# Kernel tuning notes

Measured on AMD Instinct MI355X. Metric: run time of the kernel, lower is better.

## Reference

```python
import jax, jax.numpy as jnp
import numpy as np

NUM_HEADS = 16
HEAD_DIM = 72
SCALE = HEAD_DIM ** -0.5
EPS = 1e-12


def l2norm(t):
    # torch F.normalize(dim=-1): x / norm.clamp_min(eps)
    n = jnp.sqrt(jnp.sum(t * t, axis=-1, keepdims=True))
    return t / jnp.maximum(n, EPS)


def setup_inputs() -> dict:
    key = jax.random.key(0)
    ks = jax.random.split(key, 7)
    B, N, C = 8, 1024, 1152
    x = jax.random.normal(ks[0], (B, N, C), dtype=jnp.float32)
    k_dino = jax.random.normal(ks[1], (B, NUM_HEADS, N, HEAD_DIM), dtype=jnp.float32)
    v_dino = jax.random.normal(ks[2], (B, NUM_HEADS, N, HEAD_DIM), dtype=jnp.float32)
    W_qkv = jax.random.normal(ks[3], (C, 3 * C), dtype=jnp.float32) * (C ** -0.5)
    b_qkv = jax.random.normal(ks[4], (3 * C,), dtype=jnp.float32) * 0.01
    W_proj = jax.random.normal(ks[5], (C, C), dtype=jnp.float32) * (C ** -0.5)
    b_proj = jax.random.normal(ks[6], (C,), dtype=jnp.float32) * 0.01
    return {"x": x, "k_dino": k_dino, "v_dino": v_dino,
            "W_qkv": W_qkv, "b_qkv": b_qkv, "W_proj": W_proj, "b_proj": b_proj}


def reference(x, k_dino, v_dino, W_qkv, b_qkv, W_proj, b_proj):
    # Stage 2, align_mode='logits_attn' (default path)
    B, N, C = x.shape
    qkv = (x @ W_qkv + b_qkv).reshape(B, N, 3, NUM_HEADS, HEAD_DIM)
    qkv = jnp.transpose(qkv, (2, 0, 3, 1, 4))  # [3, B, H, N, hd]
    q, k_sit, v_sit = qkv[0], qkv[1], qkv[2]   # qk_norm=False -> Identity

    # dual Q@K^T logits
    logits_dino = jnp.einsum('bhnd,bhmd->bhnm', q, k_dino) * SCALE
    logits_sit = jnp.einsum('bhnd,bhmd->bhnm', q, k_sit) * SCALE
    logits_dino_n = l2norm(logits_dino)
    logits_sit_n = l2norm(logits_sit)
    # cosine_similarity of already-unit vectors == dot product
    logit_align_loss = 1.0 - jnp.mean(jnp.sum(logits_sit_n * jax.lax.stop_gradient(logits_dino_n), axis=-1))

    attn_w_dino = jax.nn.softmax(logits_dino, axis=-1)
    attn_w_sit = jax.nn.softmax(logits_sit, axis=-1)
    attn_dino = jnp.einsum('bhnm,bhmd->bhnd', attn_w_dino, v_dino)
    attn_sit = jnp.einsum('bhnm,bhmd->bhnd', attn_w_sit, v_sit)
    attn_sit_n = l2norm(attn_sit)
    attn_dino_n = l2norm(attn_dino)
    attn_align_loss = 1.0 - jnp.mean(jnp.sum(attn_sit_n * jax.lax.stop_gradient(attn_dino_n), axis=-1))

    distill_loss = 1.0 * logit_align_loss + 0.5 * attn_align_loss

    # main attention path uses k_sit/v_sit -> identical math to attn_sit
    out = jnp.transpose(attn_sit, (0, 2, 1, 3)).reshape(B, N, C)
    out = out @ W_proj + b_proj
    return out, distill_loss
```

## Files before the change

kernel.cpp:

```cpp
#include <hip/hip_runtime.h>
#include <hip/hip_bf16.h>

typedef unsigned short bf_t;
typedef __attribute__((ext_vector_type(8))) short short8;
typedef __attribute__((ext_vector_type(4))) float f32x4;

#define B_ 8
#define H_ 16
#define N_ 1024
#define C_ 1152
#define HD 72
#define SCALE_F 0.11785113019775793f
#define EPS_F 1e-12f

typedef const __attribute__((address_space(1))) void* gas_p;
typedef __attribute__((address_space(3))) void* las_p;

__device__ inline bf_t f2bf(float f) {
  union { __hip_bfloat16 h; bf_t u; } cv;
  cv.h = __float2bfloat16(f);
  return cv.u;
}

__device__ inline void glds16(const bf_t* g, bf_t* l) {
  __builtin_amdgcn_global_load_lds((gas_p)g, (las_p)l, 16, 0, 0);
}

__global__ __launch_bounds__(256) void cast_bf16_k(const float* __restrict__ in,
                                                   bf_t* __restrict__ out, int n4) {
  int i = blockIdx.x * 256 + threadIdx.x;
  if (i < n4) {
    float4 v = reinterpret_cast<const float4*>(in)[i];
    ushort4 o;
    o.x = f2bf(v.x); o.y = f2bf(v.y); o.z = f2bf(v.z); o.w = f2bf(v.w);
    reinterpret_cast<ushort4*>(out)[i] = o;
  }
}

__global__ __launch_bounds__(256) void transpose_cast_k(const float* __restrict__ in,
                                                        bf_t* __restrict__ out, int R, int C) {
  __shared__ float t[32][33];
  const size_t bo = (size_t)blockIdx.z * R * C;
  const int tx = threadIdx.x, ty = threadIdx.y;
  const int r0 = blockIdx.y * 32, c0 = blockIdx.x * 32;
#pragma unroll
  for (int i = 0; i < 4; ++i) {
    int r = r0 + ty + i * 8, c = c0 + tx;
    if (r < R && c < C) t[ty + i * 8][tx] = in[bo + (size_t)r * C + c];
  }
  __syncthreads();
#pragma unroll
  for (int i = 0; i < 4; ++i) {
    int c = c0 + ty + i * 8, r = r0 + tx;
    if (r < R && c < C) out[bo + (size_t)c * R + r] = f2bf(t[tx][ty + i * 8]);
  }
}

template <int EPI>
__global__ __launch_bounds__(256) void gemm_bt_k(
    const bf_t* __restrict__ A, const bf_t* __restrict__ Bt,
    const float* __restrict__ bias, int K,
    bf_t* __restrict__ q_out, bf_t* __restrict__ k_out, bf_t* __restrict__ vT_out,
    float* __restrict__ f_out, int ldc) {
  __shared__ bf_t Alds[128 * 32];
  __shared__ bf_t Blds[128 * 32];
  const int tid = threadIdx.x, lane = tid & 63, wave = tid >> 6;
  const int l15 = lane & 15, l4 = lane >> 4;
  const int m0 = blockIdx.x * 128, n0 = blockIdx.y * 128;
  const int wr = (wave >> 1) * 64, wc = (wave & 1) * 64;

  f32x4 acc[4][4] = {};

  for (int k0 = 0; k0 < K; k0 += 32) {
#pragma unroll
    for (int cc = 0; cc < 2; ++cc) {
      const int c = 2 * wave + cc;
      const int idx = c * 512 + lane * 8;
      const int row = idx >> 5, col = idx & 31;
      glds16(A + (size_t)(m0 + row) * K + k0 + col, Alds + c * 512);
      glds16(Bt + (size_t)(n0 + row) * K + k0 + col, Blds + c * 512);
    }
    __syncthreads();
    short8 a[4], b[4];
#pragma unroll
    for (int i = 0; i < 4; ++i)
      a[i] = *reinterpret_cast<const short8*>(Alds + (wr + i * 16 + l15) * 32 + l4 * 8);
#pragma unroll
    for (int j = 0; j < 4; ++j)
      b[j] = *reinterpret_cast<const short8*>(Blds + (wc + j * 16 + l15) * 32 + l4 * 8);
#pragma unroll
    for (int i = 0; i < 4; ++i)
#pragma unroll
      for (int j = 0; j < 4; ++j)
        acc[i][j] = __builtin_amdgcn_mfma_f32_16x16x32_bf16(a[i], b[j], acc[i][j], 0, 0, 0);
    __syncthreads();
  }

#pragma unroll
  for (int j = 0; j < 4; ++j) {
    const int n = n0 + wc + j * 16 + l15;
    const float bn = bias[n];
    if constexpr (EPI == 0) {
      const int sec = n / C_;
      const int rem = n - sec * C_;
      const int h = rem / HD;
      const int d = rem - h * HD;
#pragma unroll
      for (int i = 0; i < 4; ++i)
#pragma unroll
        for (int r = 0; r < 4; ++r) {
          const int m = m0 + wr + i * 16 + l4 * 4 + r;
          const int bb = m >> 10, t = m & 1023;
          const float v = acc[i][j][r] + bn;
          const size_t bh = (size_t)(bb * H_ + h);
          if (sec == 0)      q_out[(bh * N_ + t) * HD + d] = f2bf(v * SCALE_F);
          else if (sec == 1) k_out[(bh * N_ + t) * HD + d] = f2bf(v);
          else               vT_out[(bh * HD + d) * N_ + t] = f2bf(v);
        }
    } else {
#pragma unroll
      for (int i = 0; i < 4; ++i)
#pragma unroll
        for (int r = 0; r < 4; ++r) {
          const int m = m0 + wr + i * 16 + l4 * 4 + r;
          f_out[(size_t)m * ldc + n] = acc[i][j][r] + bn;
        }
    }
  }
}

__global__ __launch_bounds__(256) void attn_k(
    const bf_t* __restrict__ q, const bf_t* __restrict__ ks, const bf_t* __restrict__ kd,
    const bf_t* __restrict__ vsT, const bf_t* __restrict__ vdT,
    bf_t* __restrict__ attn_out, float* __restrict__ loss_acc) {
  __shared__ bf_t Qs[64][104];
  __shared__ bf_t Ksl[64][104];
  __shared__ bf_t Kdl[64][104];
  __shared__ bf_t Vsl[80][72];
  __shared__ bf_t Vdl[80][72];
  __shared__ bf_t Pl[4][16][72];

  const int tid = threadIdx.x, lane = tid & 63, wave = tid >> 6;
  const int l15 = lane & 15, l4 = lane >> 4;
  const int bh = blockIdx.x;
  const int q0 = blockIdx.y * 64;
  const int bb = bh >> 4, h = bh & 15;

  for (int g = tid; g < 64 * 13; g += 256) {
    const int row = g / 13, cg = g % 13;
    short8 v = {};
    if (cg < 9) v = *reinterpret_cast<const short8*>(q + ((size_t)bh * N_ + q0 + row) * HD + cg * 8);
    *reinterpret_cast<short8*>(&Qs[row][cg * 8]) = v;
  }

  f32x4 S[2][4];
  f32x4 O[2][5] = {};
  f32x4 mrun[2], lrun[2], ssum, dsum, xsum;
#pragma unroll
  for (int r = 0; r < 4; ++r) {
    mrun[0][r] = -INFINITY; mrun[1][r] = -INFINITY;
    lrun[0][r] = 0.f; lrun[1][r] = 0.f;
    ssum[r] = 0.f; dsum[r] = 0.f; xsum[r] = 0.f;
  }

  for (int kt = 0; kt < 16; ++kt) {
    const int m0 = kt * 64;
    __syncthreads();
    for (int g = tid; g < 64 * 13; g += 256) {
      const int row = g / 13, cg = g % 13;
      short8 vs = {}, vd = {};
      if (cg < 9) {
        const size_t go = ((size_t)bh * N_ + m0 + row) * HD + cg * 8;
        vs = *reinterpret_cast<const short8*>(ks + go);
        vd = *reinterpret_cast<const short8*>(kd + go);
      }
      *reinterpret_cast<short8*>(&Ksl[row][cg * 8]) = vs;
      *reinterpret_cast<short8*>(&Kdl[row][cg * 8]) = vd;
    }
    for (int g = tid; g < 80 * 9; g += 256) {
      const int d = g / 9, cg = g % 9;
      short8 vs = {}, vd = {};
      if (d < HD && cg < 8) {
        const size_t go = ((size_t)bh * HD + d) * N_ + m0 + cg * 8;
        vs = *reinterpret_cast<const short8*>(vsT + go);
        vd = *reinterpret_cast<const short8*>(vdT + go);
      }
      *reinterpret_cast<short8*>(&Vsl[d][cg * 8]) = vs;
      *reinterpret_cast<short8*>(&Vdl[d][cg * 8]) = vd;
    }
    __syncthreads();

#pragma unroll
    for (int j = 0; j < 4; ++j) {
      f32x4 z = {0.f, 0.f, 0.f, 0.f};
      S[0][j] = z; S[1][j] = z;
    }
#pragma unroll
    for (int ksp = 0; ksp < 3; ++ksp) {
      const short8 aq = *reinterpret_cast<const short8*>(&Qs[wave * 16 + l15][ksp * 32 + l4 * 8]);
#pragma unroll
      for (int j = 0; j < 4; ++j) {
        const short8 b0 = *reinterpret_cast<const short8*>(&Ksl[j * 16 + l15][ksp * 32 + l4 * 8]);
        S[0][j] = __builtin_amdgcn_mfma_f32_16x16x32_bf16(aq, b0, S[0][j], 0, 0, 0);
        const short8 b1 = *reinterpret_cast<const short8*>(&Kdl[j * 16 + l15][ksp * 32 + l4 * 8]);
        S[1][j] = __builtin_amdgcn_mfma_f32_16x16x32_bf16(aq, b1, S[1][j], 0, 0, 0);
      }
    }

#pragma unroll
    for (int j = 0; j < 4; ++j)
#pragma unroll
      for (int r = 0; r < 4; ++r) {
        ssum[r] += S[0][j][r] * S[0][j][r];
        dsum[r] += S[1][j][r] * S[1][j][r];
        xsum[r] += S[0][j][r] * S[1][j][r];
      }

#pragma unroll
    for (int s = 0; s < 2; ++s) {
      f32x4 tmax;
#pragma unroll
      for (int r = 0; r < 4; ++r) {
        float t = fmaxf(fmaxf(S[s][0][r], S[s][1][r]), fmaxf(S[s][2][r], S[s][3][r]));
        t = fmaxf(t, __shfl_xor(t, 1));
        t = fmaxf(t, __shfl_xor(t, 2));
        t = fmaxf(t, __shfl_xor(t, 4));
        t = fmaxf(t, __shfl_xor(t, 8));
        tmax[r] = t;
      }
      f32x4 fac;
#pragma unroll
      for (int r = 0; r < 4; ++r) {
        const float nm = fmaxf(mrun[s][r], tmax[r]);
        fac[r] = __expf(mrun[s][r] - nm);
        mrun[s][r] = nm;
        lrun[s][r] *= fac[r];
      }
#pragma unroll
      for (int f = 0; f < 5; ++f)
#pragma unroll
        for (int r = 0; r < 4; ++r) O[s][f][r] *= fac[r];

      asm volatile("s_waitcnt lgkmcnt(0)" ::: "memory");
#pragma unroll
      for (int j = 0; j < 4; ++j)
#pragma unroll
        for (int r = 0; r < 4; ++r) {
          const float p = __expf(S[s][j][r] - mrun[s][r]);
          lrun[s][r] += p;
          Pl[wave][l4 * 4 + r][j * 16 + l15] = f2bf(p);
        }
      asm volatile("s_waitcnt lgkmcnt(0)" ::: "memory");

      const bf_t* Vp = (s == 0) ? &Vsl[0][0] : &Vdl[0][0];
#pragma unroll
      for (int k2 = 0; k2 < 2; ++k2) {
        const short8 ap = *reinterpret_cast<const short8*>(&Pl[wave][l15][k2 * 32 + l4 * 8]);
#pragma unroll
        for (int f = 0; f < 5; ++f) {
          const short8 bv = *reinterpret_cast<const short8*>(Vp + (f * 16 + l15) * HD + k2 * 32 + l4 * 8);
          O[s][f] = __builtin_amdgcn_mfma_f32_16x16x32_bf16(ap, bv, O[s][f], 0, 0, 0);
        }
      }
    }
  }

  auto red16 = [](float v) {
    v += __shfl_xor(v, 1); v += __shfl_xor(v, 2);
    v += __shfl_xor(v, 4); v += __shfl_xor(v, 8);
    return v;
  };

  float contrib = 0.f;
#pragma unroll
  for (int r = 0; r < 4; ++r) {
    const float ls = red16(lrun[0][r]);
    const float ld = red16(lrun[1][r]);
    lrun[0][r] = ls; lrun[1][r] = ld;
    const float ssR = red16(ssum[r]);
    const float ddR = red16(dsum[r]);
    const float sdR = red16(xsum[r]);
    float paa = 0.f, pbb = 0.f, pab = 0.f;
#pragma unroll
    for (int f = 0; f < 5; ++f) {
      paa += O[0][f][r] * O[0][f][r];
      pbb += O[1][f][r] * O[1][f][r];
      pab += O[0][f][r] * O[1][f][r];
    }
    const float aaR = red16(paa);
    const float bbR = red16(pbb);
    const float abR = red16(pab);
    const float cosL = sdR / (fmaxf(sqrtf(ssR), EPS_F) * fmaxf(sqrtf(ddR), EPS_F));
    const float cosA = abR / (fmaxf(sqrtf(aaR), EPS_F) * fmaxf(sqrtf(bbR), EPS_F));
    contrib += cosL + 0.5f * cosA;
  }
  if (l15 == 0) atomicAdd(loss_acc, contrib);

#pragma unroll
  for (int f = 0; f < 5; ++f) {
    const int d = f * 16 + l15;
    if (d < HD) {
#pragma unroll
      for (int r = 0; r < 4; ++r) {
        const int row = q0 + wave * 16 + l4 * 4 + r;
        const float v = O[0][f][r] / lrun[0][r];
        attn_out[(size_t)(bb * N_ + row) * C_ + h * HD + d] = f2bf(v);
      }
    }
  }
}

__global__ void finalize_k(const float* __restrict__ acc, float* __restrict__ out) {
  if (threadIdx.x == 0)
    out[(size_t)B_ * N_ * C_] = 1.5f - acc[0] * (1.0f / 131072.0f);
}

extern "C" void kernel_launch(void* const* d_in, const int* in_sizes, int n_in,
                              void* d_out, int out_size, void* d_ws, size_t ws_size,
                              hipStream_t stream) {
  const float* x      = (const float*)d_in[0];
  const float* k_dino = (const float*)d_in[1];
  const float* v_dino = (const float*)d_in[2];
  const float* W_qkv  = (const float*)d_in[3];
  const float* b_qkv  = (const float*)d_in[4];
  const float* W_proj = (const float*)d_in[5];
  const float* b_proj = (const float*)d_in[6];
  float* out = (float*)d_out;

  char* p = (char*)d_ws;
  auto alloc = [&](size_t bytes) {
    char* r = p;
    p += (bytes + 255) & ~(size_t)255;
    return r;
  };
  const size_t EL = (size_t)B_ * N_ * C_;
  bf_t* x_bf   = (bf_t*)alloc(EL * 2);
  bf_t* q_bf   = (bf_t*)alloc(EL * 2);
  bf_t* ks_bf  = (bf_t*)alloc(EL * 2);
  bf_t* kd_bf  = (bf_t*)alloc(EL * 2);
  bf_t* vsT_bf = (bf_t*)alloc(EL * 2);
  bf_t* vdT_bf = (bf_t*)alloc(EL * 2);
  bf_t* wqkvT  = (bf_t*)alloc((size_t)C_ * 3 * C_ * 2);
  bf_t* wprojT = (bf_t*)alloc((size_t)C_ * C_ * 2);
  float* loss  = (float*)alloc(256);
  bf_t* attn_bf = x_bf;

  hipMemsetAsync(loss, 0, 4, stream);
  cast_bf16_k<<<dim3((unsigned)(EL / 4 / 256)), 256, 0, stream>>>(x, x_bf, (int)(EL / 4));
  cast_bf16_k<<<dim3((unsigned)(EL / 4 / 256)), 256, 0, stream>>>(k_dino, kd_bf, (int)(EL / 4));
  transpose_cast_k<<<dim3(108, 36, 1), dim3(32, 8), 0, stream>>>(W_qkv, wqkvT, 1152, 3456);
  transpose_cast_k<<<dim3(36, 36, 1), dim3(32, 8), 0, stream>>>(W_proj, wprojT, 1152, 1152);
  transpose_cast_k<<<dim3(3, 32, 128), dim3(32, 8), 0, stream>>>(v_dino, vdT_bf, 1024, 72);
  gemm_bt_k<0><<<dim3(64, 27), 256, 0, stream>>>(x_bf, wqkvT, b_qkv, C_, q_bf, ks_bf, vsT_bf, nullptr, 0);
  attn_k<<<dim3(128, 16), 256, 0, stream>>>(q_bf, ks_bf, kd_bf, vsT_bf, vdT_bf, attn_bf, loss);
  gemm_bt_k<1><<<dim3(64, 9), 256, 0, stream>>>(attn_bf, wprojT, b_proj, C_, nullptr, nullptr, nullptr, out, C_);
  finalize_k<<<1, 64, 0, stream>>>(loss, out);
}
```

Baseline: 759.8 us.

## Restructure attention kernel: swapped MFMA operands, exp2 softmax, register Q, async K staging

Rewrites the attention kernel so Q fragments live in registers instead of LDS. S is computed transposed (K as the A operand), so each lane holds a full query column and the row max/sum needs only two cross-lane shuffles. Softmax uses exp2 with log2e folded into the Q scale, and P is written packed to LDS. K tiles are staged with global_load_lds into unpadded LDS after the barrier, overlapping the next tile's loads with loop control, and the grid order is swapped so blocks sharing a head run adjacently. In exchange the code depends on careful lane remapping for the rescale factors and loss reductions, and unpadded LDS may cause bank conflicts.

```diff
diff --git a/kernel.cpp b/kernel.cpp
--- a/kernel.cpp
+++ b/kernel.cpp
@@ -11,6 +11,7 @@
 #define C_ 1152
 #define HD 72
 #define SCALE_F 0.11785113019775793f
+#define QSC_F (SCALE_F * 1.4426950408889634f)
 #define EPS_F 1e-12f
 
 typedef const __attribute__((address_space(1))) void* gas_p;
@@ -24,6 +25,10 @@
 
 __device__ inline void glds16(const bf_t* g, bf_t* l) {
   __builtin_amdgcn_global_load_lds((gas_p)g, (las_p)l, 16, 0, 0);
+}
+
+__device__ inline f32x4 mfma32(short8 a, short8 b, f32x4 c) {
+  return __builtin_amdgcn_mfma_f32_16x16x32_bf16(a, b, c, 0, 0, 0);
 }
 
 __global__ __launch_bounds__(256) void cast_bf16_k(const float* __restrict__ in,
@@ -92,7 +97,7 @@
     for (int i = 0; i < 4; ++i)
 #pragma unroll
       for (int j = 0; j < 4; ++j)
-        acc[i][j] = __builtin_amdgcn_mfma_f32_16x16x32_bf16(a[i], b[j], acc[i][j], 0, 0, 0);
+        acc[i][j] = mfma32(a[i], b[j], acc[i][j]);
     __syncthreads();
   }
 
@@ -113,7 +118,7 @@
           const int bb = m >> 10, t = m & 1023;
           const float v = acc[i][j][r] + bn;
           const size_t bh = (size_t)(bb * H_ + h);
-          if (sec == 0)      q_out[(bh * N_ + t) * HD + d] = f2bf(v * SCALE_F);
+          if (sec == 0)      q_out[(bh * N_ + t) * HD + d] = f2bf(v * QSC_F);
           else if (sec == 1) k_out[(bh * N_ + t) * HD + d] = f2bf(v);
           else               vT_out[(bh * HD + d) * N_ + t] = f2bf(v);
         }
@@ -129,140 +134,156 @@
   }
 }
 
-__global__ __launch_bounds__(256) void attn_k(
+__global__ __launch_bounds__(256, 3) void attn_k(
     const bf_t* __restrict__ q, const bf_t* __restrict__ ks, const bf_t* __restrict__ kd,
     const bf_t* __restrict__ vsT, const bf_t* __restrict__ vdT,
     bf_t* __restrict__ attn_out, float* __restrict__ loss_acc) {
-  __shared__ bf_t Qs[64][104];
-  __shared__ bf_t Ksl[64][104];
-  __shared__ bf_t Kdl[64][104];
-  __shared__ bf_t Vsl[80][72];
-  __shared__ bf_t Vdl[80][72];
-  __shared__ bf_t Pl[4][16][72];
+  __shared__ __align__(16) bf_t SM[25344];
+  bf_t* Ksl = SM;
+  bf_t* Kdl = SM + 4608;
+  bf_t* Vsl = SM + 9216;
+  bf_t* Vdl = SM + 14976;
+  bf_t* Plb = SM + 20736;
 
   const int tid = threadIdx.x, lane = tid & 63, wave = tid >> 6;
   const int l15 = lane & 15, l4 = lane >> 4;
-  const int bh = blockIdx.x;
-  const int q0 = blockIdx.y * 64;
+  const int q0 = blockIdx.x * 64;
+  const int bh = blockIdx.y;
   const int bb = bh >> 4, h = bh & 15;
-
-  for (int g = tid; g < 64 * 13; g += 256) {
-    const int row = g / 13, cg = g % 13;
-    short8 v = {};
-    if (cg < 9) v = *reinterpret_cast<const short8*>(q + ((size_t)bh * N_ + q0 + row) * HD + cg * 8);
-    *reinterpret_cast<short8*>(&Qs[row][cg * 8]) = v;
-  }
-
-  f32x4 S[2][4];
-  f32x4 O[2][5] = {};
-  f32x4 mrun[2], lrun[2], ssum, dsum, xsum;
-#pragma unroll
-  for (int r = 0; r < 4; ++r) {
-    mrun[0][r] = -INFINITY; mrun[1][r] = -INFINITY;
-    lrun[0][r] = 0.f; lrun[1][r] = 0.f;
-    ssum[r] = 0.f; dsum[r] = 0.f; xsum[r] = 0.f;
-  }
-
+  bf_t* Plp = Plb + wave * 1152;
+
+  const int qrow = q0 + wave * 16 + l15;
+  const bf_t* qp = q + ((size_t)bh * N_ + qrow) * HD;
+  const short8 aq0 = *reinterpret_cast<const short8*>(qp + l4 * 8);
+  const short8 aq1 = *reinterpret_cast<const short8*>(qp + 32 + l4 * 8);
+  short8 aq2 = {};
+  if (l4 == 0) aq2 = *reinterpret_cast<const short8*>(qp + 64);
+
+  {
+    const short8 z = {};
+    for (int g = tid; g < 128; g += 256) {
+      const int s = g >= 64;
+      const int i = g - s * 64;
+      *reinterpret_cast<short8*>((s ? Vdl : Vsl) + (72 + (i >> 3)) * 72 + (i & 7) * 8) = z;
+    }
+  }
+
+  auto stage = [&](int m0) {
+    const size_t kbase = ((size_t)bh * N_ + m0) * HD;
+    for (int cc = wave; cc < 18; cc += 4) {
+      const int arr = (cc >= 9);
+      const int c = cc - (arr ? 9 : 0);
+      glds16((arr ? kd : ks) + kbase + c * 512 + lane * 8, (arr ? Kdl : Ksl) + c * 512);
+    }
+    for (int g = tid; g < 1152; g += 256) {
+      const int s = g >= 576;
+      const int i = g - s * 576;
+      const int row = i >> 3, cg = i & 7;
+      const short8 v = *reinterpret_cast<const short8*>(
+          (s ? vdT : vsT) + ((size_t)bh * HD + row) * N_ + m0 + cg * 8);
+      *reinterpret_cast<short8*>((s ? Vdl : Vsl) + row * 72 + cg * 8) = v;
+    }
+  };
+
+  f32x4 O0[5] = {}, O1[5] = {};
+  float m0s = -INFINITY, m1s = -INFINITY, l0s = 0.f, l1s = 0.f;
+  float ss = 0.f, dd = 0.f, xx = 0.f;
+
+  stage(0);
+
+  auto rescale = [&](f32x4 (&S)[4], f32x4 (&O)[5], float& m, float& l) {
+    float t = fmaxf(fmaxf(fmaxf(S[0][0], S[0][1]), fmaxf(S[0][2], S[0][3])),
+                    fmaxf(fmaxf(S[1][0], S[1][1]), fmaxf(S[1][2], S[1][3])));
+    t = fmaxf(t, fmaxf(fmaxf(fmaxf(S[2][0], S[2][1]), fmaxf(S[2][2], S[2][3])),
+                       fmaxf(fmaxf(S[3][0], S[3][1]), fmaxf(S[3][2], S[3][3]))));
+    t = fmaxf(t, __shfl_xor(t, 16));
+    t = fmaxf(t, __shfl_xor(t, 32));
+    const float nm = fmaxf(m, t);
+    const float fac = __builtin_amdgcn_exp2f(m - nm);
+    m = nm; l *= fac;
+    float fT[4];
+#pragma unroll
+    for (int r = 0; r < 4; ++r) fT[r] = __shfl(fac, (l4 * 4 + r) | (l4 << 4));
+#pragma unroll
+    for (int f = 0; f < 5; ++f)
+#pragma unroll
+      for (int r = 0; r < 4; ++r) O[f][r] *= fT[r];
+  };
+
+  auto write_P = [&](f32x4 (&S)[4], float m, float& l) {
+#pragma unroll
+    for (int j = 0; j < 4; ++j) {
+      const float p0 = __builtin_amdgcn_exp2f(S[j][0] - m);
+      const float p1 = __builtin_amdgcn_exp2f(S[j][1] - m);
+      const float p2 = __builtin_amdgcn_exp2f(S[j][2] - m);
+      const float p3 = __builtin_amdgcn_exp2f(S[j][3] - m);
+      l += (p0 + p1) + (p2 + p3);
+      union { __hip_bfloat162 h; unsigned u; } lo, hi;
+      lo.h = __float22bfloat162_rn(make_float2(p0, p1));
+      hi.h = __float22bfloat162_rn(make_float2(p2, p3));
+      uint2 w; w.x = lo.u; w.y = hi.u;
+      *reinterpret_cast<uint2*>(Plp + l15 * 72 + j * 16 + l4 * 4) = w;
+    }
+  };
+
+  auto pv = [&](f32x4 (&O)[5], const bf_t* Vp) {
+#pragma unroll
+    for (int k2 = 0; k2 < 2; ++k2) {
+      const short8 ap = *reinterpret_cast<const short8*>(Plp + l15 * 72 + k2 * 32 + l4 * 8);
+#pragma unroll
+      for (int f = 0; f < 5; ++f) {
+        const short8 bv = *reinterpret_cast<const short8*>(
+            Vp + (f * 16 + l15) * HD + k2 * 32 + l4 * 8);
+        O[f] = mfma32(ap, bv, O[f]);
+      }
+    }
+  };
+
+#pragma unroll 1
   for (int kt = 0; kt < 16; ++kt) {
-    const int m0 = kt * 64;
     __syncthreads();
-    for (int g = tid; g < 64 * 13; g += 256) {
-      const int row = g / 13, cg = g % 13;
-      short8 vs = {}, vd = {};
-      if (cg < 9) {
-        const size_t go = ((size_t)bh * N_ + m0 + row) * HD + cg * 8;
-        vs = *reinterpret_cast<const short8*>(ks + go);
-        vd = *reinterpret_cast<const short8*>(kd + go);
+
+    f32x4 S0[4] = {}, S1[4] = {};
+#pragma unroll
+    for (int ksp = 0; ksp < 2; ++ksp) {
+      const short8 qf = ksp ? aq1 : aq0;
+#pragma unroll
+      for (int j = 0; j < 4; ++j) {
+        const int ko = (j * 16 + l15) * HD + ksp * 32 + l4 * 8;
+        S0[j] = mfma32(*reinterpret_cast<const short8*>(Ksl + ko), qf, S0[j]);
+        S1[j] = mfma32(*reinterpret_cast<const short8*>(Kdl + ko), qf, S1[j]);
       }
-      *reinterpret_cast<short8*>(&Ksl[row][cg * 8]) = vs;
-      *reinterpret_cast<short8*>(&Kdl[row][cg * 8]) = vd;
-    }
-    for (int g = tid; g < 80 * 9; g += 256) {
-      const int d = g / 9, cg = g % 9;
-      short8 vs = {}, vd = {};
-      if (d < HD && cg < 8) {
-        const size_t go = ((size_t)bh * HD + d) * N_ + m0 + cg * 8;
-        vs = *reinterpret_cast<const short8*>(vsT + go);
-        vd = *reinterpret_cast<const short8*>(vdT + go);
+    }
+#pragma unroll
+    for (int j = 0; j < 4; ++j) {
+      const int ko = (j * 16 + l15) * HD + 64 + l4 * 8;
+      S0[j] = mfma32(*reinterpret_cast<const short8*>(Ksl + ko), aq2, S0[j]);
+      S1[j] = mfma32(*reinterpret_cast<const short8*>(Kdl + ko), aq2, S1[j]);
+    }
+
+#pragma unroll
+    for (int j = 0; j < 4; ++j)
+#pragma unroll
+      for (int r = 0; r < 4; ++r) {
+        ss += S0[j][r] * S0[j][r];
+        dd += S1[j][r] * S1[j][r];
+        xx += S0[j][r] * S1[j][r];
       }
-      *reinterpret_cast<short8*>(&Vsl[d][cg * 8]) = vs;
-      *reinterpret_cast<short8*>(&Vdl[d][cg * 8]) = vd;
-    }
+
+    rescale(S0, O0, m0s, l0s);
+    asm volatile("s_waitcnt lgkmcnt(0)" ::: "memory");
+    write_P(S0, m0s, l0s);
+    asm volatile("s_waitcnt lgkmcnt(0)" ::: "memory");
+    pv(O0, Vsl);
+
+    rescale(S1, O1, m1s, l1s);
+    asm volatile("s_waitcnt lgkmcnt(0)" ::: "memory");
+    write_P(S1, m1s, l1s);
+    asm volatile("s_waitcnt lgkmcnt(0)" ::: "memory");
+    pv(O1, Vdl);
+
     __syncthreads();
-
-#pragma unroll
-    for (int j = 0; j < 4; ++j) {
-      f32x4 z = {0.f, 0.f, 0.f, 0.f};
-      S[0][j] = z; S[1][j] = z;
-    }
-#pragma unroll
-    for (int ksp = 0; ksp < 3; ++ksp) {
-      const short8 aq = *reinterpret_cast<const short8*>(&Qs[wave * 16 + l15][ksp * 32 + l4 * 8]);
-#pragma unroll
-      for (int j = 0; j < 4; ++j) {
-        const short8 b0 = *reinterpret_cast<const short8*>(&Ksl[j * 16 + l15][ksp * 32 + l4 * 8]);
-        S[0][j] = __builtin_amdgcn_mfma_f32_16x16x32_bf16(aq, b0, S[0][j], 0, 0, 0);
-        const short8 b1 = *reinterpret_cast<const short8*>(&Kdl[j * 16 + l15][ksp * 32 + l4 * 8]);
-        S[1][j] = __builtin_amdgcn_mfma_f32_16x16x32_bf16(aq, b1, S[1][j], 0, 0, 0);
-      }
-    }
-
-#pragma unroll
-    for (int j = 0; j < 4; ++j)
-#pragma unroll
-      for (int r = 0; r < 4; ++r) {
-        ssum[r] += S[0][j][r] * S[0][j][r];
-        dsum[r] += S[1][j][r] * S[1][j][r];
-        xsum[r] += S[0][j][r] * S[1][j][r];
-      }
-
-#pragma unroll
-    for (int s = 0; s < 2; ++s) {
-      f32x4 tmax;
-#pragma unroll
-      for (int r = 0; r < 4; ++r) {
-        float t = fmaxf(fmaxf(S[s][0][r], S[s][1][r]), fmaxf(S[s][2][r], S[s][3][r]));
-        t = fmaxf(t, __shfl_xor(t, 1));
-        t = fmaxf(t, __shfl_xor(t, 2));
-        t = fmaxf(t, __shfl_xor(t, 4));
-        t = fmaxf(t, __shfl_xor(t, 8));
-        tmax[r] = t;
-      }
-      f32x4 fac;
-#pragma unroll
-      for (int r = 0; r < 4; ++r) {
-        const float nm = fmaxf(mrun[s][r], tmax[r]);
-        fac[r] = __expf(mrun[s][r] - nm);
-        mrun[s][r] = nm;
-        lrun[s][r] *= fac[r];
-      }
-#pragma unroll
-      for (int f = 0; f < 5; ++f)
-#pragma unroll
-        for (int r = 0; r < 4; ++r) O[s][f][r] *= fac[r];
-
-      asm volatile("s_waitcnt lgkmcnt(0)" ::: "memory");
-#pragma unroll
-      for (int j = 0; j < 4; ++j)
-#pragma unroll
-        for (int r = 0; r < 4; ++r) {
-          const float p = __expf(S[s][j][r] - mrun[s][r]);
-          lrun[s][r] += p;
-          Pl[wave][l4 * 4 + r][j * 16 + l15] = f2bf(p);
-        }
-      asm volatile("s_waitcnt lgkmcnt(0)" ::: "memory");
-
-      const bf_t* Vp = (s == 0) ? &Vsl[0][0] : &Vdl[0][0];
-#pragma unroll
-      for (int k2 = 0; k2 < 2; ++k2) {
-        const short8 ap = *reinterpret_cast<const short8*>(&Pl[wave][l15][k2 * 32 + l4 * 8]);
-#pragma unroll
-        for (int f = 0; f < 5; ++f) {
-          const short8 bv = *reinterpret_cast<const short8*>(Vp + (f * 16 + l15) * HD + k2 * 32 + l4 * 8);
-          O[s][f] = __builtin_amdgcn_mfma_f32_16x16x32_bf16(ap, bv, O[s][f], 0, 0, 0);
-        }
-      }
-    }
+    if (kt < 15) stage((kt + 1) * 64);
   }
 
   auto red16 = [](float v) {
@@ -270,32 +291,36 @@
     v += __shfl_xor(v, 4); v += __shfl_xor(v, 8);
     return v;
   };
-
-  float contrib = 0.f;
+  auto redL4 = [](float v) {
+    v += __shfl_xor(v, 16); v += __shfl_xor(v, 32);
+    return v;
+  };
+
+  const float ssT = redL4(ss), ddT = redL4(dd), xxT = redL4(xx);
+  const float lsT = redL4(l0s);
+  const float cosL = xxT / (fmaxf(sqrtf(ssT), EPS_F) * fmaxf(sqrtf(ddT), EPS_F));
+  const float sumL = red16(cosL);
+
+  float sumA = 0.f;
 #pragma unroll
   for (int r = 0; r < 4; ++r) {
-    const float ls = red16(lrun[0][r]);
-    const float ld = red16(lrun[1][r]);
-    lrun[0][r] = ls; lrun[1][r] = ld;
-    const float ssR = red16(ssum[r]);
-    const float ddR = red16(dsum[r]);
-    const float sdR = red16(xsum[r]);
-    float paa = 0.f, pbb = 0.f, pab = 0.f;
+    float aa = 0.f, bb2 = 0.f, ab = 0.f;
 #pragma unroll
     for (int f = 0; f < 5; ++f) {
-      paa += O[0][f][r] * O[0][f][r];
-      pbb += O[1][f][r] * O[1][f][r];
-      pab += O[0][f][r] * O[1][f][r];
-    }
-    const float aaR = red16(paa);
-    const float bbR = red16(pbb);
-    const float abR = red16(pab);
-    const float cosL = sdR / (fmaxf(sqrtf(ssR), EPS_F) * fmaxf(sqrtf(ddR), EPS_F));
-    const float cosA = abR / (fmaxf(sqrtf(aaR), EPS_F) * fmaxf(sqrtf(bbR), EPS_F));
-    contrib += cosL + 0.5f * cosA;
-  }
-  if (l15 == 0) atomicAdd(loss_acc, contrib);
-
+      const float w = (f < 4 || l15 < 8) ? 1.f : 0.f;
+      const float a = O0[f][r], b = O1[f][r];
+      aa += w * a * a; bb2 += w * b * b; ab += w * a * b;
+    }
+    aa = red16(aa); bb2 = red16(bb2); ab = red16(ab);
+    sumA += ab / (fmaxf(sqrtf(aa), EPS_F) * fmaxf(sqrtf(bb2), EPS_F));
+  }
+  sumA = redL4(sumA);
+
+  if (lane == 0) atomicAdd(loss_acc, sumL + 0.5f * sumA);
+
+  float lT[4];
+#pragma unroll
+  for (int r = 0; r < 4; ++r) lT[r] = __shfl(lsT, (l4 * 4 + r) | (l4 << 4));
 #pragma unroll
   for (int f = 0; f < 5; ++f) {
     const int d = f * 16 + l15;
@@ -303,8 +328,7 @@
 #pragma unroll
       for (int r = 0; r < 4; ++r) {
         const int row = q0 + wave * 16 + l4 * 4 + r;
-        const float v = O[0][f][r] / lrun[0][r];
-        attn_out[(size_t)(bb * N_ + row) * C_ + h * HD + d] = f2bf(v);
+        attn_out[(size_t)(bb * N_ + row) * C_ + h * HD + d] = f2bf(O0[f][r] / lT[r]);
       }
     }
   }
@@ -352,7 +376,7 @@
   transpose_cast_k<<<dim3(36, 36, 1), dim3(32, 8), 0, stream>>>(W_proj, wprojT, 1152, 1152);
   transpose_cast_k<<<dim3(3, 32, 128), dim3(32, 8), 0, stream>>>(v_dino, vdT_bf, 1024, 72);
   gemm_bt_k<0><<<dim3(64, 27), 256, 0, stream>>>(x_bf, wqkvT, b_qkv, C_, q_bf, ks_bf, vsT_bf, nullptr, 0);
-  attn_k<<<dim3(128, 16), 256, 0, stream>>>(q_bf, ks_bf, kd_bf, vsT_bf, vdT_bf, attn_bf, loss);
+  attn_k<<<dim3(16, 128), 256, 0, stream>>>(q_bf, ks_bf, kd_bf, vsT_bf, vdT_bf, attn_bf, loss);
   gemm_bt_k<1><<<dim3(64, 9), 256, 0, stream>>>(attn_bf, wprojT, b_proj, C_, nullptr, nullptr, nullptr, out, C_);
   finalize_k<<<1, 64, 0, stream>>>(loss, out);
 }
```

Result: faster. 621.6 us (-18.2%).
